# Optimization experiments

Measured on AMD Instinct MI355X. Metric: run time of the kernel, lower is better.

## Reference

```python
import jax, jax.numpy as jnp
import numpy as np

QN, QP = -8, 7  # signed 4-bit


def round_pass(x):
    # straight-through round (forward: round-half-even like torch.round)
    return x + jax.lax.stop_gradient(jnp.round(x) - x)


def setup_inputs() -> dict:
    key = jax.random.key(0)
    ks = jax.random.split(key, 9)
    B, S, D, H = 16, 1024, 768, 3072
    def unif(k, shape):
        return jax.random.uniform(k, shape, jnp.float32, 0.02, 0.1)
    return {
        "x0": jax.random.normal(ks[0], (B, S, D), jnp.float32),
        "w1": jax.random.normal(ks[1], (H, D), jnp.float32) * 0.02,
        "b1": jax.random.normal(ks[2], (H,), jnp.float32) * 0.02,
        "alpha_w1": unif(ks[3], (H,)),
        "alpha_a1": unif(ks[4], (D,)),
        "w2": jax.random.normal(ks[5], (D, H), jnp.float32) * 0.02,
        "b2": jax.random.normal(ks[6], (D,), jnp.float32) * 0.02,
        "alpha_w2": unif(ks[7], (D,)),
        "alpha_a2": unif(ks[8], (H,)),
    }


def _quant_act(x, alpha_a):
    # ActQ_v2: per-tensor (mean of kernel-wise alpha), signed int4
    a = alpha_a.mean()
    return round_pass(jnp.clip(x / a, QN, QP))


def _quant_w(w, alpha_w):
    # LinearQ_v2: per-output-channel alpha, shape [out, in]
    return round_pass(jnp.clip(w / alpha_w[:, None], QN, QP))


def reference(x0, w1, b1, alpha_w1, alpha_a1, w2, b2, alpha_w2, alpha_a2):
    # fc1: int4 act quant, int4 weight quant, integer matmul, dequant scale + bias
    xq = _quant_act(x0, alpha_a1)                       # [B,S,D] integer-valued
    wq1 = _quant_w(w1, alpha_w1)                        # [H,D] integer-valued
    x1 = jnp.einsum('bsd,hd->bsh', xq, wq1)             # int matmul (float carrier)
    x1 = x1 * alpha_w1 * alpha_a1.mean() + b1           # per-channel dequant + bias
    x1 = jax.nn.gelu(x1, approximate=False)             # nn.GELU (exact erf)
    x1 = jnp.clip(x1, -10.0, 10.0)
    # dropout p=0.0 -> identity
    # fc2
    hq = _quant_act(x1, alpha_a2)                       # [B,S,H]
    wq2 = _quant_w(w2, alpha_w2)                        # [D,H]
    x2 = jnp.einsum('bsh,dh->bsd', hq, wq2)
    x2 = x2 * alpha_w2 * alpha_a2.mean() + b2
    return x2
```

## Files before the change

### kernel.cpp

```cpp
#include <hip/hip_runtime.h>
#include <hip/hip_bf16.h>
#include <math.h>


typedef __attribute__((ext_vector_type(4))) int i32x4;

__device__ __forceinline__ void gload_lds16(const void* g, void* l) {
  __builtin_amdgcn_global_load_lds(
      (const __attribute__((address_space(1))) void*)g,
      (__attribute__((address_space(3))) void*)l, 16, 0, 0);
}

__device__ __forceinline__ int q4_i8(float x, float a) {
  float t = x / a;
  t = fminf(fmaxf(t, -8.0f), 7.0f);
  t = rintf(t);
  return (int)t;
}

__global__ void means_k(const float* __restrict__ v1, int n1,
                        const float* __restrict__ v2, int n2,
                        float* __restrict__ out) {
  const float* src = blockIdx.x ? v2 : v1;
  const int n = blockIdx.x ? n2 : n1;
  __shared__ double red[256];
  double s = 0.0;
  for (int i = threadIdx.x; i < n; i += 256) s += (double)src[i];
  red[threadIdx.x] = s;
  __syncthreads();
  for (int st = 128; st > 0; st >>= 1) {
    if (threadIdx.x < st) red[threadIdx.x] += red[threadIdx.x + st];
    __syncthreads();
  }
  if (threadIdx.x == 0) {
    float m = (float)(red[0] / (double)n);
    out[blockIdx.x] = m;
    if (blockIdx.x == 1) {
      out[2] = 1.0f / m;
      out[3] = 0.5f * (1.0f / m);
    }
  }
}

__global__ void quant_x_k(const float* __restrict__ x,
                          unsigned* __restrict__ xq,
                          const float* __restrict__ means, int n4) {
  int i = blockIdx.x * blockDim.x + threadIdx.x;
  if (i >= n4) return;
  const float a = means[0];
  float4 v = ((const float4*)x)[i];
  unsigned u = (q4_i8(v.x, a) & 0xFF) | ((q4_i8(v.y, a) & 0xFF) << 8) |
               ((q4_i8(v.z, a) & 0xFF) << 16) | ((q4_i8(v.w, a) & 0xFF) << 24);
  xq[i] = u;
}

__global__ void quant_w_k(const float* __restrict__ w,
                          const float* __restrict__ alpha,
                          unsigned* __restrict__ wq, int C, int n4) {
  int i = blockIdx.x * blockDim.x + threadIdx.x;
  if (i >= n4) return;
  int row = (i * 4) / C;
  const float a = alpha[row];
  float4 v = ((const float4*)w)[i];
  unsigned u = (q4_i8(v.x, a) & 0xFF) | ((q4_i8(v.y, a) & 0xFF) << 8) |
               ((q4_i8(v.z, a) & 0xFF) << 16) | ((q4_i8(v.w, a) & 0xFF) << 24);
  wq[i] = u;
}

template <int EPI>
__global__ __launch_bounds__(256, 2) void gemm_k(
    const signed char* __restrict__ A, const signed char* __restrict__ B,
    const float* __restrict__ alphaw, const float* __restrict__ bias,
    const float* __restrict__ means, signed char* __restrict__ out_b,
    float* __restrict__ out_f, int N, int K) {
  __shared__ __align__(16) signed char sA0[128 * 128];
  __shared__ __align__(16) signed char sB0[128 * 128];
  __shared__ __align__(16) signed char sA1[128 * 128];
  __shared__ __align__(16) signed char sB1[128 * 128];
  const int tid = threadIdx.x;
  const int w = tid >> 6;
  const int l = tid & 63;
  const int wm = w >> 1, wn = w & 1;
  const long bm0 = (long)blockIdx.y * 128;
  const long bn0 = (long)blockIdx.x * 128;

  i32x4 acc[4][4] = {};

  const int srow = l >> 3;
  const int scol = ((l & 7) * 16) ^ (srow << 4);
  const int rsw = (l & 7) << 4;

  const signed char* gA = A + (bm0 + (w * 4) * 8 + srow) * (long)K + scol;
  const signed char* gB = B + (bn0 + (w * 4) * 8 + srow) * (long)K + scol;

  auto STAGE = [&](signed char* dA, signed char* dB, int kt) {
#pragma unroll
    for (int i = 0; i < 4; ++i) {
      gload_lds16(gA + (long)i * 8 * K + kt, dA + (w * 4 + i) * 1024);
      gload_lds16(gB + (long)i * 8 * K + kt, dB + (w * 4 + i) * 1024);
    }
  };
  auto COMPUTE = [&](const signed char* pA, const signed char* pB) {
#pragma unroll
    for (int kk = 0; kk < 2; ++kk) {
      const int kc = (kk * 64 + (l >> 4) * 16) ^ rsw;
      i32x4 af[4], bg[4];
#pragma unroll
      for (int m = 0; m < 4; ++m)
        af[m] = *(const i32x4*)&pA[(wm * 64 + m * 16 + (l & 15)) * 128 + kc];
#pragma unroll
      for (int n = 0; n < 4; ++n)
        bg[n] = *(const i32x4*)&pB[(wn * 64 + n * 16 + (l & 15)) * 128 + kc];
#pragma unroll
      for (int m = 0; m < 4; ++m)
#pragma unroll
        for (int n = 0; n < 4; ++n)
          acc[m][n] = __builtin_amdgcn_mfma_i32_16x16x64_i8(af[m], bg[n],
                                                            acc[m][n], 0, 0, 0);
    }
  };

  const int nt = K >> 7;
  STAGE(sA0, sB0, 0);
  __syncthreads();
  for (int t = 0; t < nt; t += 2) {
    if (t + 1 < nt) STAGE(sA1, sB1, (t + 1) << 7);
    COMPUTE(sA0, sB0);
    __syncthreads();
    if (t + 2 < nt) STAGE(sA0, sB0, (t + 2) << 7);
    COMPUTE(sA1, sB1);
    __syncthreads();
  }

  const float a1 = means[0];
  const float a2 = means[1];
  const float half_inv_a2 = means[3];

  float awc[4], bsc[4];
  const int cc0 = (int)bn0 + wn * 64 + (l & 15);
#pragma unroll
  for (int n = 0; n < 4; ++n) {
    awc[n] = alphaw[cc0 + n * 16];
    bsc[n] = bias[cc0 + n * 16];
  }

  const int r0 = (int)bm0 + wm * 64 + (l >> 4) * 4;

  if (EPI == 1) {
    float awa1[4];
#pragma unroll
    for (int n = 0; n < 4; ++n) awa1[n] = awc[n] * a1;
#pragma unroll
    for (int m = 0; m < 4; ++m) {
#pragma unroll
      for (int rg = 0; rg < 4; ++rg) {
        const int r = r0 + m * 16 + rg;
        signed char* prow = out_b + (size_t)r * N + cc0;
#pragma unroll
        for (int n = 0; n < 4; ++n) {
          const float f = (float)acc[m][n][rg];
          const float t = fmaf(f, awa1[n], bsc[n]);
          const float x = t * 0.70710678118654752f;
          const float az = fabsf(x);
          const float rr = __builtin_amdgcn_rcpf(fmaf(0.3275911f, az, 1.0f));
          float p = fmaf(rr, 1.061405429f, -1.453152027f);
          p = fmaf(rr, p, 1.421413741f);
          p = fmaf(rr, p, -0.284496736f);
          p = fmaf(rr, p, 0.254829592f);
          p = p * rr;
          const float e = __expf(-az * az);
          float er = fmaf(-p, e, 1.0f);
          er = copysignf(er, x);
          float qv = t * (1.0f + er) * half_inv_a2;
          qv = fminf(fmaxf(qv, -8.0f), 7.0f);
          qv = rintf(qv);
          prow[n * 16] = (signed char)(int)qv;
        }
      }
    }
  } else {
#pragma unroll
    for (int m = 0; m < 4; ++m) {
#pragma unroll
      for (int rg = 0; rg < 4; ++rg) {
        const int r = r0 + m * 16 + rg;
        float* prow = out_f + (size_t)r * N + cc0;
#pragma unroll
        for (int n = 0; n < 4; ++n) {
          const float f = (float)acc[m][n][rg];
          float t = __fmul_rn(f, awc[n]);
          t = __fmul_rn(t, a2);
          t = __fadd_rn(t, bsc[n]);
          prow[n * 16] = t;
        }
      }
    }
  }
}

extern "C" void kernel_launch(void* const* d_in, const int* in_sizes, int n_in,
                              void* d_out, int out_size, void* d_ws,
                              size_t ws_size, hipStream_t stream) {
  const float* x0 = (const float*)d_in[0];
  const float* w1 = (const float*)d_in[1];
  const float* b1 = (const float*)d_in[2];
  const float* aw1 = (const float*)d_in[3];
  const float* aa1 = (const float*)d_in[4];
  const float* w2 = (const float*)d_in[5];
  const float* b2 = (const float*)d_in[6];
  const float* aw2 = (const float*)d_in[7];
  const float* aa2 = (const float*)d_in[8];

  char* ws = (char*)d_ws;
  float* means = (float*)ws;
  signed char* xq = (signed char*)(ws + 256);
  signed char* wq1 = (signed char*)(ws + 12583168);
  signed char* wq2 = (signed char*)(ws + 14942464);
  signed char* hq = (signed char*)(ws + 17301760);

  means_k<<<2, 256, 0, stream>>>(aa1, 768, aa2, 3072, means);
  quant_x_k<<<12288, 256, 0, stream>>>(x0, (unsigned*)xq, means, 3145728);
  quant_w_k<<<2304, 256, 0, stream>>>(w1, aw1, (unsigned*)wq1, 768, 589824);
  quant_w_k<<<2304, 256, 0, stream>>>(w2, aw2, (unsigned*)wq2, 3072, 589824);
  dim3 g1(24, 128);
  gemm_k<1><<<g1, 256, 0, stream>>>(xq, wq1, aw1, b1, means, hq, nullptr, 3072,
                                    768);
  dim3 g2(6, 128);
  gemm_k<2><<<g2, 256, 0, stream>>>(hq, wq2, aw2, b2, means, nullptr,
                                    (float*)d_out, 768, 3072);
}
```

Before: 149.5 us.

## Use 512-thread GEMM blocks with 64-wide K tiles and smaller per-wave tiles

The int8 GEMM now runs 8 waves per 128x128 block instead of 4, with each wave covering a 32x64 sub-tile. The K tile shrinks from 128 to 64 with a new LDS swizzle, so each block uses 32KB of LDS instead of 64KB. With launch bounds of (512, 6) the intent is more resident waves per CU to hide latency. In exchange there are twice as many barriers per unit of K, less reuse of A/B fragments per wave, and a tighter register budget.

```diff
diff --git a/kernel.cpp b/kernel.cpp
--- a/kernel.cpp
+++ b/kernel.cpp
@@ -68,15 +68,15 @@
 }
 
 template <int EPI>
-__global__ __launch_bounds__(256, 2) void gemm_k(
+__global__ __launch_bounds__(512, 6) void gemm_k(
     const signed char* __restrict__ A, const signed char* __restrict__ B,
     const float* __restrict__ alphaw, const float* __restrict__ bias,
     const float* __restrict__ means, signed char* __restrict__ out_b,
     float* __restrict__ out_f, int N, int K) {
-  __shared__ __align__(16) signed char sA0[128 * 128];
-  __shared__ __align__(16) signed char sB0[128 * 128];
-  __shared__ __align__(16) signed char sA1[128 * 128];
-  __shared__ __align__(16) signed char sB1[128 * 128];
+  __shared__ __align__(16) signed char sA0[128 * 64];
+  __shared__ __align__(16) signed char sB0[128 * 64];
+  __shared__ __align__(16) signed char sA1[128 * 64];
+  __shared__ __align__(16) signed char sB1[128 * 64];
   const int tid = threadIdx.x;
   const int w = tid >> 6;
   const int l = tid & 63;
@@ -84,50 +84,42 @@
   const long bm0 = (long)blockIdx.y * 128;
   const long bn0 = (long)blockIdx.x * 128;
 
-  i32x4 acc[4][4] = {};
-
-  const int srow = l >> 3;
-  const int scol = ((l & 7) * 16) ^ (srow << 4);
-  const int rsw = (l & 7) << 4;
-
-  const signed char* gA = A + (bm0 + (w * 4) * 8 + srow) * (long)K + scol;
-  const signed char* gB = B + (bn0 + (w * 4) * 8 + srow) * (long)K + scol;
+  i32x4 acc[2][4] = {};
+
+  const int srow = l >> 2;
+  const int scol = (((l & 3) ^ (srow & 3)) << 4);
+  const int rsw = ((l >> 4) ^ (l & 3)) << 4;
+
+  const signed char* gA = A + (bm0 + w * 16 + srow) * (long)K + scol;
+  const signed char* gB = B + (bn0 + w * 16 + srow) * (long)K + scol;
 
   auto STAGE = [&](signed char* dA, signed char* dB, int kt) {
-#pragma unroll
-    for (int i = 0; i < 4; ++i) {
-      gload_lds16(gA + (long)i * 8 * K + kt, dA + (w * 4 + i) * 1024);
-      gload_lds16(gB + (long)i * 8 * K + kt, dB + (w * 4 + i) * 1024);
-    }
+    gload_lds16(gA + kt, dA + w * 1024);
+    gload_lds16(gB + kt, dB + w * 1024);
   };
   auto COMPUTE = [&](const signed char* pA, const signed char* pB) {
-#pragma unroll
-    for (int kk = 0; kk < 2; ++kk) {
-      const int kc = (kk * 64 + (l >> 4) * 16) ^ rsw;
-      i32x4 af[4], bg[4];
-#pragma unroll
-      for (int m = 0; m < 4; ++m)
-        af[m] = *(const i32x4*)&pA[(wm * 64 + m * 16 + (l & 15)) * 128 + kc];
+    i32x4 af[2], bg[4];
+#pragma unroll
+    for (int m = 0; m < 2; ++m)
+      af[m] = *(const i32x4*)&pA[(wm * 32 + m * 16 + (l & 15)) * 64 + rsw];
+#pragma unroll
+    for (int n = 0; n < 4; ++n)
+      bg[n] = *(const i32x4*)&pB[(wn * 64 + n * 16 + (l & 15)) * 64 + rsw];
+#pragma unroll
+    for (int m = 0; m < 2; ++m)
 #pragma unroll
       for (int n = 0; n < 4; ++n)
-        bg[n] = *(const i32x4*)&pB[(wn * 64 + n * 16 + (l & 15)) * 128 + kc];
-#pragma unroll
-      for (int m = 0; m < 4; ++m)
-#pragma unroll
-        for (int n = 0; n < 4; ++n)
-          acc[m][n] = __builtin_amdgcn_mfma_i32_16x16x64_i8(af[m], bg[n],
-                                                            acc[m][n], 0, 0, 0);
-    }
+        acc[m][n] = __builtin_amdgcn_mfma_i32_16x16x64_i8(af[m], bg[n],
+                                                          acc[m][n], 0, 0, 0);
   };
 
-  const int nt = K >> 7;
   STAGE(sA0, sB0, 0);
   __syncthreads();
-  for (int t = 0; t < nt; t += 2) {
-    if (t + 1 < nt) STAGE(sA1, sB1, (t + 1) << 7);
+  for (int kt = 0; kt < K; kt += 128) {
+    STAGE(sA1, sB1, kt + 64);
     COMPUTE(sA0, sB0);
     __syncthreads();
-    if (t + 2 < nt) STAGE(sA0, sB0, (t + 2) << 7);
+    if (kt + 128 < K) STAGE(sA0, sB0, kt + 128);
     COMPUTE(sA1, sB1);
     __syncthreads();
   }
@@ -144,14 +136,14 @@
     bsc[n] = bias[cc0 + n * 16];
   }
 
-  const int r0 = (int)bm0 + wm * 64 + (l >> 4) * 4;
+  const int r0 = (int)bm0 + wm * 32 + (l >> 4) * 4;
 
   if (EPI == 1) {
     float awa1[4];
 #pragma unroll
     for (int n = 0; n < 4; ++n) awa1[n] = awc[n] * a1;
 #pragma unroll
-    for (int m = 0; m < 4; ++m) {
+    for (int m = 0; m < 2; ++m) {
 #pragma unroll
       for (int rg = 0; rg < 4; ++rg) {
         const int r = r0 + m * 16 + rg;
@@ -180,7 +172,7 @@
     }
   } else {
 #pragma unroll
-    for (int m = 0; m < 4; ++m) {
+    for (int m = 0; m < 2; ++m) {
 #pragma unroll
       for (int rg = 0; rg < 4; ++rg) {
         const int r = r0 + m * 16 + rg;
@@ -223,9 +215,9 @@
   quant_w_k<<<2304, 256, 0, stream>>>(w1, aw1, (unsigned*)wq1, 768, 589824);
   quant_w_k<<<2304, 256, 0, stream>>>(w2, aw2, (unsigned*)wq2, 3072, 589824);
   dim3 g1(24, 128);
-  gemm_k<1><<<g1, 256, 0, stream>>>(xq, wq1, aw1, b1, means, hq, nullptr, 3072,
+  gemm_k<1><<<g1, 512, 0, stream>>>(xq, wq1, aw1, b1, means, hq, nullptr, 3072,
                                     768);
   dim3 g2(6, 128);
-  gemm_k<2><<<g2, 256, 0, stream>>>(hq, wq2, aw2, b2, means, nullptr,
+  gemm_k<2><<<g2, 512, 0, stream>>>(hq, wq2, aw2, b2, means, nullptr,
                                     (float*)d_out, 768, 3072);
 }
```

Result: no change. 151.6 us (+1.4%).
